# Kernel tuning notes

Hardware: AMD Instinct MI355X
Metric: run time of the kernel (lower is better)

## Reference

```python
import jax, jax.numpy as jnp
import numpy as np

N = 50000   # num_nodes
E = 800000  # num edges (COO)
T = 50      # timesteps
H = 64      # hidden_units


def setup_inputs() -> dict:
    key = jax.random.key(0)
    ks = jax.random.split(key, 16)
    s = 0.1  # weight init scale
    return {
        "features": jax.random.normal(ks[0], (1, T, N), jnp.float32),
        "index": jax.random.randint(ks[1], (E, 2), 0, N, jnp.int32),
        "value": jax.random.uniform(ks[2], (E,), jnp.float32),
        "W1_g": jax.random.normal(ks[3], (1 + H, 2 * H), jnp.float32) * s,
        "b1_g": jnp.ones((2 * H,), jnp.float32),
        "W1_c": jax.random.normal(ks[4], (1 + H, H), jnp.float32) * s,
        "b1_c": jnp.zeros((H,), jnp.float32),
        "W2b_g": jax.random.normal(ks[5], (H + 1, 2), jnp.float32) * s,
        "b2b_g": jnp.ones((2,), jnp.float32),
        "W2b_c": jax.random.normal(ks[6], (H + 1, 1), jnp.float32) * s,
        "b2b_c": jnp.zeros((1,), jnp.float32),
        "W2u_g": jax.random.normal(ks[7], (H + 1, 2), jnp.float32) * s,
        "b2u_g": jnp.ones((2,), jnp.float32),
        "W2u_c": jax.random.normal(ks[8], (H + 1, 1), jnp.float32) * s,
        "b2u_c": jnp.zeros((1,), jnp.float32),
    }


def _spmm(rows, cols, vals, X):
    # sparse COO adjacency (rows, cols, vals) @ dense X [N, d]
    return jax.ops.segment_sum(vals[:, None] * X[cols], rows, num_segments=N)


def _gru_layer(xs, rows, cols, vals, Wg, bg, Wc, bc, units):
    # xs: [T, N, d_in]; GCN-GRU cell scanned over time, batch=1
    h0 = jnp.zeros((N, units), xs.dtype)

    def step(h, x):
        def gconv(st, W, b):
            xc = jnp.concatenate([x, st], axis=-1)     # [N, d_in+units]
            return _spmm(rows, cols, vals, xc) @ W + b  # [N, out]

        ru = jax.nn.sigmoid(gconv(h, Wg, bg))
        r, u = jnp.split(ru, 2, axis=-1)
        c = jnp.tanh(gconv(r * h, Wc, bc))
        hn = u * h + (1.0 - u) * c
        return hn, hn

    _, hs = jax.lax.scan(step, h0, xs)
    return hs  # [T, N, units]


def reference(features, index, value, W1_g, b1_g, W1_c, b1_c,
              W2b_g, b2b_g, W2b_c, b2b_c, W2u_g, b2u_g, W2u_c, b2u_c):
    rows, cols = index[:, 0], index[:, 1]
    xs = features[0][..., None]  # [T, N, 1]
    # shared first layer (cell_1 is used by both multi-cell stacks)
    h1 = _gru_layer(xs, rows, cols, value, W1_g, b1_g, W1_c, b1_c, H)  # [T,N,H]
    out_b = _gru_layer(h1, rows, cols, value, W2b_g, b2b_g, W2b_c, b2b_c, 1)
    out_u = _gru_layer(h1, rows, cols, value, W2u_g, b2u_g, W2u_c, b2u_c, 1)
    # dynamic_rnn outputs: [batch=1, T, N]
    return out_b[..., 0][None], out_u[..., 0][None]
```

## Files before the change

kernel.cpp:

```cpp
#include <hip/hip_runtime.h>
#include <math.h>

#define NN 50000
#define EE 800000
#define TT 50
#define EVCAP 1150016
#define SB 196

__device__ __forceinline__ float sigm(float x)   { return 1.f / (1.f + __expf(-x)); }
__device__ __forceinline__ float tanh_f(float x) { float e = __expf(2.f * x); return 1.f - 2.f / (e + 1.f); }


__global__ __launch_bounds__(256) void hist_kernel(const int* __restrict__ idx, int* __restrict__ cnt) {
    int e = blockIdx.x * blockDim.x + threadIdx.x;
    if (e < EE) atomicAdd(&cnt[idx[2 * e]], 1);
}

__global__ __launch_bounds__(256) void scan1(const int* __restrict__ cnt, int* __restrict__ rp,
                                             int* __restrict__ bsum) {
    __shared__ int s[256];
    int t = threadIdx.x;
    int g = blockIdx.x * 256 + t;
    int v = (g < NN) ? ((cnt[g] + 7) & ~7) : 0;
    s[t] = v;
    __syncthreads();
    for (int off = 1; off < 256; off <<= 1) {
        int add = (t >= off) ? s[t - off] : 0;
        __syncthreads();
        v += add;
        s[t] = v;
        __syncthreads();
    }
    if (g < NN) rp[g + 1] = v;
    if (t == 255) bsum[blockIdx.x] = v;
}

__global__ __launch_bounds__(256) void scan2(int* __restrict__ bsum) {
    __shared__ int s[256];
    int t = threadIdx.x;
    int v = (t < SB) ? bsum[t] : 0;
    s[t] = v;
    __syncthreads();
    for (int off = 1; off < 256; off <<= 1) {
        int add = (t >= off) ? s[t - off] : 0;
        __syncthreads();
        v += add;
        s[t] = v;
        __syncthreads();
    }
    if (t < SB) bsum[t] = v;
}

__global__ __launch_bounds__(256) void scan3(int* __restrict__ rp, const int* __restrict__ bsum) {
    int g = blockIdx.x * 256 + threadIdx.x;
    int off = (blockIdx.x > 0) ? bsum[blockIdx.x - 1] : 0;
    if (g < NN) rp[g + 1] += off;
    if (g == 0) rp[0] = 0;
}

__global__ __launch_bounds__(256) void scatter_kernel(const int* __restrict__ idx, const float* __restrict__ val,
                                                      const int* __restrict__ rp, int* __restrict__ cnt,
                                                      int2* __restrict__ ev) {
    int e = blockIdx.x * blockDim.x + threadIdx.x;
    if (e >= EE) return;
    int r = idx[2 * e];
    int p = rp[r] + atomicAdd(&cnt[r], 1);
    ev[p] = make_int2(idx[2 * e + 1], __float_as_int(val[e]));
}


__global__ __launch_bounds__(256) void transpose_x(const float* __restrict__ F, float* __restrict__ xT) {
    __shared__ float tile[64][51];
    int n0 = blockIdx.x * 64;
    for (int i = threadIdx.x; i < TT * 64; i += 256) {
        int t = i >> 6, n = i & 63;
        if (n0 + n < NN) tile[n][t] = F[(size_t)t * NN + n0 + n];
    }
    __syncthreads();
    for (int i = threadIdx.x; i < 64 * 64; i += 256) {
        int n = i >> 6, t = i & 63;
        if (n0 + n < NN) xT[(size_t)(n0 + n) * 64 + t] = (t < TT) ? tile[n][t] : 0.f;
    }
}

__global__ __launch_bounds__(256) void spmm_sx(const int* __restrict__ rp, const int2* __restrict__ ev,
                                               const float* __restrict__ xT, float* __restrict__ SxAll) {
    int w = __builtin_amdgcn_readfirstlane((blockIdx.x * blockDim.x + threadIdx.x) >> 6);
    int lane = threadIdx.x & 63;
    if (w >= NN) return;
    int e  = __builtin_amdgcn_readfirstlane(rp[w]);
    int e1 = __builtin_amdgcn_readfirstlane(rp[w + 1]);
    const float* xl = xT + lane;
    float a0 = 0.f, a1 = 0.f, a2 = 0.f, a3 = 0.f, a4 = 0.f, a5 = 0.f, a6 = 0.f, a7 = 0.f;
    for (; e < e1; e += 8) {
        int2 q0 = ev[e + 0], q1 = ev[e + 1], q2 = ev[e + 2], q3 = ev[e + 3];
        int2 q4 = ev[e + 4], q5 = ev[e + 5], q6 = ev[e + 6], q7 = ev[e + 7];
        a0 = fmaf(__int_as_float(q0.y), xl[(size_t)q0.x * 64], a0);
        a1 = fmaf(__int_as_float(q1.y), xl[(size_t)q1.x * 64], a1);
        a2 = fmaf(__int_as_float(q2.y), xl[(size_t)q2.x * 64], a2);
        a3 = fmaf(__int_as_float(q3.y), xl[(size_t)q3.x * 64], a3);
        a4 = fmaf(__int_as_float(q4.y), xl[(size_t)q4.x * 64], a4);
        a5 = fmaf(__int_as_float(q5.y), xl[(size_t)q5.x * 64], a5);
        a6 = fmaf(__int_as_float(q6.y), xl[(size_t)q6.x * 64], a6);
        a7 = fmaf(__int_as_float(q7.y), xl[(size_t)q7.x * 64], a7);
    }
    float s = ((a0 + a1) + (a2 + a3)) + ((a4 + a5) + (a6 + a7));
    if (lane < TT) SxAll[(size_t)lane * NN + w] = s;
}


__global__ __launch_bounds__(256) void spmm_cand(const int* __restrict__ rp, const int2* __restrict__ ev,
        const float* __restrict__ rh, const float* __restrict__ Sx,
        const float* __restrict__ Wc, const float* __restrict__ bc,
        const float* __restrict__ u1, float* __restrict__ h1,
        const float* __restrict__ Wbg, const float* __restrict__ Wbc,
        const float* __restrict__ Wug, const float* __restrict__ Wuc,
        float* __restrict__ z8) {
    __shared__ float ldsW[65 * 64];
    __shared__ float ldsS[4][64];
    int t = threadIdx.x;
    for (int i = t; i < 65 * 16; i += 256)
        ((float4*)ldsW)[i] = ((const float4*)Wc)[i];
    __syncthreads();
    int lane = t & 63;
    int wv = t >> 6;
    int j = lane;
    float bj = bc[j];
    float wz0 = Wbg[j * 2], wz1 = Wbg[j * 2 + 1], wz2 = Wbc[j];
    float wz3 = Wug[j * 2], wz4 = Wug[j * 2 + 1], wz5 = Wuc[j];
    int wstride = gridDim.x * 4;
    for (int wi = blockIdx.x * 4 + wv; wi < NN; wi += wstride) {
        int w = __builtin_amdgcn_readfirstlane(wi);
        int e  = __builtin_amdgcn_readfirstlane(rp[w]);
        int e1 = __builtin_amdgcn_readfirstlane(rp[w + 1]);
        const float* xl = rh + lane;
        float a0 = 0.f, a1 = 0.f, a2 = 0.f, a3 = 0.f, a4 = 0.f, a5 = 0.f, a6 = 0.f, a7 = 0.f;
        for (; e < e1; e += 8) {
            int2 q0 = ev[e + 0], q1 = ev[e + 1], q2 = ev[e + 2], q3 = ev[e + 3];
            int2 q4 = ev[e + 4], q5 = ev[e + 5], q6 = ev[e + 6], q7 = ev[e + 7];
            a0 = fmaf(__int_as_float(q0.y), xl[(size_t)q0.x * 64], a0);
            a1 = fmaf(__int_as_float(q1.y), xl[(size_t)q1.x * 64], a1);
            a2 = fmaf(__int_as_float(q2.y), xl[(size_t)q2.x * 64], a2);
            a3 = fmaf(__int_as_float(q3.y), xl[(size_t)q3.x * 64], a3);
            a4 = fmaf(__int_as_float(q4.y), xl[(size_t)q4.x * 64], a4);
            a5 = fmaf(__int_as_float(q5.y), xl[(size_t)q5.x * 64], a5);
            a6 = fmaf(__int_as_float(q6.y), xl[(size_t)q6.x * 64], a6);
            a7 = fmaf(__int_as_float(q7.y), xl[(size_t)q7.x * 64], a7);
        }
        float s2 = ((a0 + a1) + (a2 + a3)) + ((a4 + a5) + (a6 + a7));
        ldsS[wv][lane] = s2;
        float acc = fmaf(Sx[w], ldsW[j], bj);
#pragma unroll 8
        for (int k = 0; k < 64; ++k)
            acc = fmaf(ldsS[wv][k], ldsW[(k + 1) * 64 + j], acc);
        float c = tanh_f(acc);
        float u  = u1[(size_t)w * 64 + j];
        float ho = h1[(size_t)w * 64 + j];
        float hn = fmaf(u, ho - c, c);
        h1[(size_t)w * 64 + j] = hn;
        float p0 = hn * wz0, p1 = hn * wz1, p2 = hn * wz2;
        float p3 = hn * wz3, p4 = hn * wz4, p5 = hn * wz5;
#pragma unroll
        for (int off = 1; off < 64; off <<= 1) {
            p0 += __shfl_xor(p0, off);
            p1 += __shfl_xor(p1, off);
            p2 += __shfl_xor(p2, off);
            p3 += __shfl_xor(p3, off);
            p4 += __shfl_xor(p4, off);
            p5 += __shfl_xor(p5, off);
        }
        if (j == 0) {
            z8[(size_t)w * 8 + 0] = p0; z8[(size_t)w * 8 + 1] = p1; z8[(size_t)w * 8 + 2] = p2;
            z8[(size_t)w * 8 + 3] = p3; z8[(size_t)w * 8 + 4] = p4; z8[(size_t)w * 8 + 5] = p5;
        }
    }
}


__global__ __launch_bounds__(256) void merged1(int GA,
        const int* __restrict__ rp, const int2* __restrict__ ev,
        const float* __restrict__ h1, float* __restrict__ Sh,
        const float* __restrict__ z8,
        const float* __restrict__ hb, const float* __restrict__ hu,
        const float* __restrict__ Wbg, const float* __restrict__ bbg,
        const float* __restrict__ Wug, const float* __restrict__ bug,
        float* __restrict__ z2, float* __restrict__ g2, float* __restrict__ S3c) {
    if ((int)blockIdx.x < GA) {
        int w = __builtin_amdgcn_readfirstlane(((int)blockIdx.x * 256 + (int)threadIdx.x) >> 6);
        int lane = threadIdx.x & 63;
        if (w >= NN) return;
        int e  = __builtin_amdgcn_readfirstlane(rp[w]);
        int e1 = __builtin_amdgcn_readfirstlane(rp[w + 1]);
        const float* xl = h1 + lane;
        float a0 = 0.f, a1 = 0.f, a2 = 0.f, a3 = 0.f, a4 = 0.f, a5 = 0.f, a6 = 0.f, a7 = 0.f;
        for (; e < e1; e += 8) {
            int2 q0 = ev[e + 0], q1 = ev[e + 1], q2 = ev[e + 2], q3 = ev[e + 3];
            int2 q4 = ev[e + 4], q5 = ev[e + 5], q6 = ev[e + 6], q7 = ev[e + 7];
            a0 = fmaf(__int_as_float(q0.y), xl[(size_t)q0.x * 64], a0);
            a1 = fmaf(__int_as_float(q1.y), xl[(size_t)q1.x * 64], a1);
            a2 = fmaf(__int_as_float(q2.y), xl[(size_t)q2.x * 64], a2);
            a3 = fmaf(__int_as_float(q3.y), xl[(size_t)q3.x * 64], a3);
            a4 = fmaf(__int_as_float(q4.y), xl[(size_t)q4.x * 64], a4);
            a5 = fmaf(__int_as_float(q5.y), xl[(size_t)q5.x * 64], a5);
            a6 = fmaf(__int_as_float(q6.y), xl[(size_t)q6.x * 64], a6);
            a7 = fmaf(__int_as_float(q7.y), xl[(size_t)q7.x * 64], a7);
        }
        Sh[(size_t)w * 64 + lane] = ((a0 + a1) + (a2 + a3)) + ((a4 + a5) + (a6 + a7));
    } else {
        int gid = ((int)blockIdx.x - GA) * 256 + threadIdx.x;
        int row = gid >> 3;
        int j = gid & 7;
        if (row >= NN) return;
        int e = rp[row], e1 = rp[row + 1];
        float a0 = 0.f, a1 = 0.f, a2 = 0.f, a3 = 0.f;
        for (; e + 3 < e1; e += 4) {
            int2 p0 = ev[e], p1 = ev[e + 1], p2 = ev[e + 2], p3 = ev[e + 3];
            a0 = fmaf(__int_as_float(p0.y), z8[(size_t)p0.x * 8 + j], a0);
            a1 = fmaf(__int_as_float(p1.y), z8[(size_t)p1.x * 8 + j], a1);
            a2 = fmaf(__int_as_float(p2.y), z8[(size_t)p2.x * 8 + j], a2);
            a3 = fmaf(__int_as_float(p3.y), z8[(size_t)p3.x * 8 + j], a3);
        }
        for (; e < e1; ++e) {
            int2 p = ev[e];
            a0 = fmaf(__int_as_float(p.y), z8[(size_t)p.x * 8 + j], a0);
        }
        float s = (a0 + a1) + (a2 + a3);
        if (j == 2) S3c[row * 2 + 0] = s;
        if (j == 5) S3c[row * 2 + 1] = s;
        int lane = threadIdx.x & 63;
        int base = lane & ~7;
        float s0 = __shfl(s, base + 0);
        float s1 = __shfl(s, base + 1);
        float s3 = __shfl(s, base + 3);
        float s4 = __shfl(s, base + 4);
        float s6 = __shfl(s, base + 6);
        float s7 = __shfl(s, base + 7);
        if (j == 0) {
            float rb = sigm(fmaf(s6, Wbg[128], s0) + bbg[0]);
            float ub = sigm(fmaf(s6, Wbg[129], s1) + bbg[1]);
            float ru = sigm(fmaf(s7, Wug[128], s3) + bug[0]);
            float uu = sigm(fmaf(s7, Wug[129], s4) + bug[1]);
            z2[row * 2 + 0] = rb * hb[row];
            z2[row * 2 + 1] = ru * hu[row];
            g2[row * 2 + 0] = ub;
            g2[row * 2 + 1] = uu;
        }
    }
}


#define G1_CHUNK 32
__global__ __launch_bounds__(128) void merged2(int GA,
        const float* __restrict__ Sh, const float* __restrict__ Sx,
        const float* __restrict__ Wg, const float* __restrict__ bg,
        const float* __restrict__ h1, float* __restrict__ rh, float* __restrict__ u1,
        const int* __restrict__ rp, const int2* __restrict__ ev,
        const float* __restrict__ z2, const float* __restrict__ S3c, const float* __restrict__ g2,
        const float* __restrict__ Wbc, const float* __restrict__ bbc,
        const float* __restrict__ Wuc, const float* __restrict__ buc,
        float* __restrict__ hb, float* __restrict__ hu,
        float* __restrict__ z8, float* __restrict__ out, int tPrev) {
    __shared__ float4 s4[G1_CHUNK][16];
    __shared__ float sxl[G1_CHUNK];
    if ((int)blockIdx.x < GA) {
        int j = threadIdx.x;
        float w0 = Wg[j];
        float wk[64];
#pragma unroll
        for (int k = 0; k < 64; ++k) wk[k] = Wg[(1 + k) * 128 + j];
        float bj = bg[j];
        int n0 = (int)blockIdx.x * G1_CHUNK;
        int nmax = min(G1_CHUNK, NN - n0);
        for (int idx = j; idx < G1_CHUNK * 16; idx += 128) {
            int n = idx >> 4, q = idx & 15;
            if (n < nmax) s4[n][q] = *(const float4*)(Sh + (size_t)(n0 + n) * 64 + q * 4);
        }
        if (j < G1_CHUNK && j < nmax) sxl[j] = Sx[n0 + j];
        __syncthreads();
        for (int n = 0; n < nmax; ++n) {
            float acc = fmaf(sxl[n], w0, bj);
#pragma unroll
            for (int q = 0; q < 16; ++q) {
                float4 sv = s4[n][q];
                acc = fmaf(sv.x, wk[4 * q + 0], acc);
                acc = fmaf(sv.y, wk[4 * q + 1], acc);
                acc = fmaf(sv.z, wk[4 * q + 2], acc);
                acc = fmaf(sv.w, wk[4 * q + 3], acc);
            }
            float g = sigm(acc);
            int node = n0 + n;
            if (j < 64) rh[(size_t)node * 64 + j] = g * h1[(size_t)node * 64 + j];
            else        u1[(size_t)node * 64 + (j - 64)] = g;
        }
    } else {
        int gid = ((int)blockIdx.x - GA) * 128 + threadIdx.x;
        int row = gid >> 1;
        int j = gid & 1;
        if (row >= NN) return;
        int e = rp[row], e1 = rp[row + 1];
        float a0 = 0.f, a1 = 0.f, a2 = 0.f, a3 = 0.f;
        for (; e + 3 < e1; e += 4) {
            int2 p0 = ev[e], p1 = ev[e + 1], p2 = ev[e + 2], p3 = ev[e + 3];
            a0 = fmaf(__int_as_float(p0.y), z2[(size_t)p0.x * 2 + j], a0);
            a1 = fmaf(__int_as_float(p1.y), z2[(size_t)p1.x * 2 + j], a1);
            a2 = fmaf(__int_as_float(p2.y), z2[(size_t)p2.x * 2 + j], a2);
            a3 = fmaf(__int_as_float(p3.y), z2[(size_t)p3.x * 2 + j], a3);
        }
        for (; e < e1; ++e) {
            int2 p = ev[e];
            a0 = fmaf(__int_as_float(p.y), z2[(size_t)p.x * 2 + j], a0);
        }
        float s = (a0 + a1) + (a2 + a3);
        int lane = threadIdx.x & 63;
        int base = lane & ~1;
        float sA = __shfl(s, base + 0);
        float sB = __shfl(s, base + 1);
        if (j == 0) {
            float cb = tanh_f(fmaf(sA, Wbc[64], S3c[row * 2 + 0]) + bbc[0]);
            float cu = tanh_f(fmaf(sB, Wuc[64], S3c[row * 2 + 1]) + buc[0]);
            float ub = g2[row * 2 + 0], uu = g2[row * 2 + 1];
            float hbn = fmaf(ub, hb[row] - cb, cb);
            float hun = fmaf(uu, hu[row] - cu, cu);
            hb[row] = hbn; hu[row] = hun;
            z8[(size_t)row * 8 + 6] = hbn;
            z8[(size_t)row * 8 + 7] = hun;
            out[(size_t)tPrev * NN + row] = hbn;
            out[(size_t)(TT + tPrev) * NN + row] = hun;
        }
    }
}


extern "C" void kernel_launch(void* const* d_in, const int* in_sizes, int n_in,
                              void* d_out, int out_size, void* d_ws, size_t ws_size,
                              hipStream_t stream) {
    const float* features = (const float*)d_in[0];
    const int*   index    = (const int*)d_in[1];
    const float* value    = (const float*)d_in[2];
    const float* W1g  = (const float*)d_in[3];
    const float* b1g  = (const float*)d_in[4];
    const float* W1c  = (const float*)d_in[5];
    const float* b1c  = (const float*)d_in[6];
    const float* W2bg = (const float*)d_in[7];
    const float* b2bg = (const float*)d_in[8];
    const float* W2bc = (const float*)d_in[9];
    const float* b2bc = (const float*)d_in[10];
    const float* W2ug = (const float*)d_in[11];
    const float* b2ug = (const float*)d_in[12];
    const float* W2uc = (const float*)d_in[13];
    const float* b2uc = (const float*)d_in[14];
    float* out = (float*)d_out;

    char* ws = (char*)d_ws;
    size_t o = 0;
    auto alloc = [&](size_t bytes) { size_t cur = o; o += (bytes + 255) & ~(size_t)255; return cur; };
    size_t o_h1  = alloc((size_t)NN * 64 * 4);
    size_t o_hb  = alloc((size_t)NN * 4);
    size_t o_hu  = alloc((size_t)NN * 4);
    size_t o_z8  = alloc((size_t)NN * 8 * 4);
    size_t zeroEnd = o;
    size_t o_rp  = alloc((size_t)(NN + 1) * 4);
    size_t o_cnt = alloc((size_t)NN * 4);
    size_t o_bs  = alloc((size_t)256 * 4);
    size_t o_ev  = alloc((size_t)EVCAP * 8);
    size_t o_Sh  = alloc((size_t)NN * 64 * 4);
    size_t o_SxA = alloc((size_t)TT * NN * 4);
    size_t o_rh  = alloc((size_t)NN * 64 * 4);
    size_t o_u1  = alloc((size_t)NN * 64 * 4);
    size_t o_S3c = alloc((size_t)NN * 2 * 4);
    size_t o_z2  = alloc((size_t)NN * 2 * 4);
    size_t o_g2  = alloc((size_t)NN * 2 * 4);
    (void)ws_size; (void)in_sizes; (void)n_in; (void)out_size;

    float* h1  = (float*)(ws + o_h1);
    float* hb  = (float*)(ws + o_hb);
    float* hu  = (float*)(ws + o_hu);
    float* z8  = (float*)(ws + o_z8);
    int*   rp  = (int*)(ws + o_rp);
    int*   cnt = (int*)(ws + o_cnt);
    int*   bsum = (int*)(ws + o_bs);
    int2*  ev  = (int2*)(ws + o_ev);
    float* Sh  = (float*)(ws + o_Sh);
    float* SxA = (float*)(ws + o_SxA);
    float* rh  = (float*)(ws + o_rh);
    float* u1  = (float*)(ws + o_u1);
    float* S3c = (float*)(ws + o_S3c);
    float* z2  = (float*)(ws + o_z2);
    float* g2  = (float*)(ws + o_g2);
    float* xT  = rh;

    (void)hipMemsetAsync(ws + o_cnt, 0, (size_t)NN * 4, stream);
    hist_kernel<<<(EE + 255) / 256, 256, 0, stream>>>(index, cnt);
    scan1<<<SB, 256, 0, stream>>>(cnt, rp, bsum);
    scan2<<<1, 256, 0, stream>>>(bsum);
    scan3<<<SB, 256, 0, stream>>>(rp, bsum);
    (void)hipMemsetAsync(ws + o_cnt, 0, (size_t)NN * 4, stream);
    (void)hipMemsetAsync(ws + o_ev, 0, (size_t)EVCAP * 8, stream);
    scatter_kernel<<<(EE + 255) / 256, 256, 0, stream>>>(index, value, rp, cnt, ev);

    (void)hipMemsetAsync(ws + o_h1, 0, zeroEnd - o_h1, stream);
    (void)hipMemsetAsync(ws + o_Sh, 0, (size_t)NN * 64 * 4, stream);

    transpose_x<<<(NN + 63) / 64, 256, 0, stream>>>(features, xT);
    spmm_sx<<<(NN + 3) / 4, 256, 0, stream>>>(rp, ev, xT, SxA);

    const int GA1 = (NN + 3) / 4;
    const int GB1 = (NN * 8 + 255) / 256;
    const int GA2 = (NN + G1_CHUNK - 1) / G1_CHUNK;
    const int GB2 = (NN * 2 + 127) / 128;

    for (int t = 0; t < TT; ++t) {
        const float* Sxt = SxA + (size_t)t * NN;
        int g2grid = (t > 0) ? (GA2 + GB2) : GA2;
        merged2<<<g2grid, 128, 0, stream>>>(GA2, Sh, Sxt, W1g, b1g, h1, rh, u1,
                                            rp, ev, z2, S3c, g2, W2bc, b2bc, W2uc, b2uc,
                                            hb, hu, z8, out, t - 1);
        spmm_cand<<<2048, 256, 0, stream>>>(rp, ev, rh, Sxt, W1c, b1c, u1, h1,
                                            W2bg, W2bc, W2ug, W2uc, z8);
        int gA = (t < TT - 1) ? GA1 : 0;
        merged1<<<gA + GB1, 256, 0, stream>>>(gA, rp, ev, h1, Sh,
                                              z8, hb, hu, W2bg, b2bg, W2ug, b2ug, z2, g2, S3c);
    }
    merged2<<<GB2, 128, 0, stream>>>(0, Sh, SxA, W1g, b1g, h1, rh, u1,
                                     rp, ev, z2, S3c, g2, W2bc, b2bc, W2uc, b2uc,
                                     hb, hu, z8, out, TT - 1);
}
```

Before: 6.255 ms.

## Unroll gathers to 16 edges and restructure gate GEMV to persistent 256-thread blocks

```diff
diff --git a/kernel.cpp b/kernel.cpp
--- a/kernel.cpp
+++ b/kernel.cpp
@@ -83,6 +83,45 @@
     }
 }
 
+#define GATH16(TBL)                                                                   \
+    float a0=0.f,a1=0.f,a2=0.f,a3=0.f,a4=0.f,a5=0.f,a6=0.f,a7=0.f;                    \
+    float b0=0.f,b1=0.f,b2=0.f,b3=0.f,b4=0.f,b5=0.f,b6=0.f,b7=0.f;                    \
+    for (; e + 16 <= e1; e += 16) {                                                   \
+        int2 q0=ev[e+0],q1=ev[e+1],q2=ev[e+2],q3=ev[e+3];                             \
+        int2 q4=ev[e+4],q5=ev[e+5],q6=ev[e+6],q7=ev[e+7];                             \
+        int2 r0=ev[e+8],r1=ev[e+9],r2=ev[e+10],r3=ev[e+11];                           \
+        int2 r4=ev[e+12],r5=ev[e+13],r6=ev[e+14],r7=ev[e+15];                         \
+        a0=fmaf(__int_as_float(q0.y),TBL[(size_t)q0.x*64],a0);                        \
+        a1=fmaf(__int_as_float(q1.y),TBL[(size_t)q1.x*64],a1);                        \
+        a2=fmaf(__int_as_float(q2.y),TBL[(size_t)q2.x*64],a2);                        \
+        a3=fmaf(__int_as_float(q3.y),TBL[(size_t)q3.x*64],a3);                        \
+        a4=fmaf(__int_as_float(q4.y),TBL[(size_t)q4.x*64],a4);                        \
+        a5=fmaf(__int_as_float(q5.y),TBL[(size_t)q5.x*64],a5);                        \
+        a6=fmaf(__int_as_float(q6.y),TBL[(size_t)q6.x*64],a6);                        \
+        a7=fmaf(__int_as_float(q7.y),TBL[(size_t)q7.x*64],a7);                        \
+        b0=fmaf(__int_as_float(r0.y),TBL[(size_t)r0.x*64],b0);                        \
+        b1=fmaf(__int_as_float(r1.y),TBL[(size_t)r1.x*64],b1);                        \
+        b2=fmaf(__int_as_float(r2.y),TBL[(size_t)r2.x*64],b2);                        \
+        b3=fmaf(__int_as_float(r3.y),TBL[(size_t)r3.x*64],b3);                        \
+        b4=fmaf(__int_as_float(r4.y),TBL[(size_t)r4.x*64],b4);                        \
+        b5=fmaf(__int_as_float(r5.y),TBL[(size_t)r5.x*64],b5);                        \
+        b6=fmaf(__int_as_float(r6.y),TBL[(size_t)r6.x*64],b6);                        \
+        b7=fmaf(__int_as_float(r7.y),TBL[(size_t)r7.x*64],b7);                        \
+    }                                                                                 \
+    if (e < e1) {                                                 \
+        int2 q0=ev[e+0],q1=ev[e+1],q2=ev[e+2],q3=ev[e+3];                             \
+        int2 q4=ev[e+4],q5=ev[e+5],q6=ev[e+6],q7=ev[e+7];                             \
+        a0=fmaf(__int_as_float(q0.y),TBL[(size_t)q0.x*64],a0);                        \
+        a1=fmaf(__int_as_float(q1.y),TBL[(size_t)q1.x*64],a1);                        \
+        a2=fmaf(__int_as_float(q2.y),TBL[(size_t)q2.x*64],a2);                        \
+        a3=fmaf(__int_as_float(q3.y),TBL[(size_t)q3.x*64],a3);                        \
+        a4=fmaf(__int_as_float(q4.y),TBL[(size_t)q4.x*64],a4);                        \
+        a5=fmaf(__int_as_float(q5.y),TBL[(size_t)q5.x*64],a5);                        \
+        a6=fmaf(__int_as_float(q6.y),TBL[(size_t)q6.x*64],a6);                        \
+        a7=fmaf(__int_as_float(q7.y),TBL[(size_t)q7.x*64],a7);                        \
+    }                                                                                 \
+    float rsum = (((a0+a1)+(a2+a3))+((a4+a5)+(a6+a7))) + (((b0+b1)+(b2+b3))+((b4+b5)+(b6+b7)));
+
 __global__ __launch_bounds__(256) void spmm_sx(const int* __restrict__ rp, const int2* __restrict__ ev,
                                                const float* __restrict__ xT, float* __restrict__ SxAll) {
     int w = __builtin_amdgcn_readfirstlane((blockIdx.x * blockDim.x + threadIdx.x) >> 6);
@@ -91,21 +130,8 @@
     int e  = __builtin_amdgcn_readfirstlane(rp[w]);
     int e1 = __builtin_amdgcn_readfirstlane(rp[w + 1]);
     const float* xl = xT + lane;
-    float a0 = 0.f, a1 = 0.f, a2 = 0.f, a3 = 0.f, a4 = 0.f, a5 = 0.f, a6 = 0.f, a7 = 0.f;
-    for (; e < e1; e += 8) {
-        int2 q0 = ev[e + 0], q1 = ev[e + 1], q2 = ev[e + 2], q3 = ev[e + 3];
-        int2 q4 = ev[e + 4], q5 = ev[e + 5], q6 = ev[e + 6], q7 = ev[e + 7];
-        a0 = fmaf(__int_as_float(q0.y), xl[(size_t)q0.x * 64], a0);
-        a1 = fmaf(__int_as_float(q1.y), xl[(size_t)q1.x * 64], a1);
-        a2 = fmaf(__int_as_float(q2.y), xl[(size_t)q2.x * 64], a2);
-        a3 = fmaf(__int_as_float(q3.y), xl[(size_t)q3.x * 64], a3);
-        a4 = fmaf(__int_as_float(q4.y), xl[(size_t)q4.x * 64], a4);
-        a5 = fmaf(__int_as_float(q5.y), xl[(size_t)q5.x * 64], a5);
-        a6 = fmaf(__int_as_float(q6.y), xl[(size_t)q6.x * 64], a6);
-        a7 = fmaf(__int_as_float(q7.y), xl[(size_t)q7.x * 64], a7);
-    }
-    float s = ((a0 + a1) + (a2 + a3)) + ((a4 + a5) + (a6 + a7));
-    if (lane < TT) SxAll[(size_t)lane * NN + w] = s;
+    GATH16(xl)
+    if (lane < TT) SxAll[(size_t)lane * NN + w] = rsum;
 }
 
 
@@ -134,21 +160,8 @@
         int e  = __builtin_amdgcn_readfirstlane(rp[w]);
         int e1 = __builtin_amdgcn_readfirstlane(rp[w + 1]);
         const float* xl = rh + lane;
-        float a0 = 0.f, a1 = 0.f, a2 = 0.f, a3 = 0.f, a4 = 0.f, a5 = 0.f, a6 = 0.f, a7 = 0.f;
-        for (; e < e1; e += 8) {
-            int2 q0 = ev[e + 0], q1 = ev[e + 1], q2 = ev[e + 2], q3 = ev[e + 3];
-            int2 q4 = ev[e + 4], q5 = ev[e + 5], q6 = ev[e + 6], q7 = ev[e + 7];
-            a0 = fmaf(__int_as_float(q0.y), xl[(size_t)q0.x * 64], a0);
-            a1 = fmaf(__int_as_float(q1.y), xl[(size_t)q1.x * 64], a1);
-            a2 = fmaf(__int_as_float(q2.y), xl[(size_t)q2.x * 64], a2);
-            a3 = fmaf(__int_as_float(q3.y), xl[(size_t)q3.x * 64], a3);
-            a4 = fmaf(__int_as_float(q4.y), xl[(size_t)q4.x * 64], a4);
-            a5 = fmaf(__int_as_float(q5.y), xl[(size_t)q5.x * 64], a5);
-            a6 = fmaf(__int_as_float(q6.y), xl[(size_t)q6.x * 64], a6);
-            a7 = fmaf(__int_as_float(q7.y), xl[(size_t)q7.x * 64], a7);
-        }
-        float s2 = ((a0 + a1) + (a2 + a3)) + ((a4 + a5) + (a6 + a7));
-        ldsS[wv][lane] = s2;
+        GATH16(xl)
+        ldsS[wv][lane] = rsum;
         float acc = fmaf(Sx[w], ldsW[j], bj);
 #pragma unroll 8
         for (int k = 0; k < 64; ++k)
@@ -192,39 +205,28 @@
         int e  = __builtin_amdgcn_readfirstlane(rp[w]);
         int e1 = __builtin_amdgcn_readfirstlane(rp[w + 1]);
         const float* xl = h1 + lane;
-        float a0 = 0.f, a1 = 0.f, a2 = 0.f, a3 = 0.f, a4 = 0.f, a5 = 0.f, a6 = 0.f, a7 = 0.f;
-        for (; e < e1; e += 8) {
-            int2 q0 = ev[e + 0], q1 = ev[e + 1], q2 = ev[e + 2], q3 = ev[e + 3];
-            int2 q4 = ev[e + 4], q5 = ev[e + 5], q6 = ev[e + 6], q7 = ev[e + 7];
-            a0 = fmaf(__int_as_float(q0.y), xl[(size_t)q0.x * 64], a0);
-            a1 = fmaf(__int_as_float(q1.y), xl[(size_t)q1.x * 64], a1);
-            a2 = fmaf(__int_as_float(q2.y), xl[(size_t)q2.x * 64], a2);
-            a3 = fmaf(__int_as_float(q3.y), xl[(size_t)q3.x * 64], a3);
-            a4 = fmaf(__int_as_float(q4.y), xl[(size_t)q4.x * 64], a4);
-            a5 = fmaf(__int_as_float(q5.y), xl[(size_t)q5.x * 64], a5);
-            a6 = fmaf(__int_as_float(q6.y), xl[(size_t)q6.x * 64], a6);
-            a7 = fmaf(__int_as_float(q7.y), xl[(size_t)q7.x * 64], a7);
-        }
-        Sh[(size_t)w * 64 + lane] = ((a0 + a1) + (a2 + a3)) + ((a4 + a5) + (a6 + a7));
+        GATH16(xl)
+        Sh[(size_t)w * 64 + lane] = rsum;
     } else {
         int gid = ((int)blockIdx.x - GA) * 256 + threadIdx.x;
         int row = gid >> 3;
         int j = gid & 7;
         if (row >= NN) return;
         int e = rp[row], e1 = rp[row + 1];
-        float a0 = 0.f, a1 = 0.f, a2 = 0.f, a3 = 0.f;
-        for (; e + 3 < e1; e += 4) {
+        float a0 = 0.f, a1 = 0.f, a2 = 0.f, a3 = 0.f, a4 = 0.f, a5 = 0.f, a6 = 0.f, a7 = 0.f;
+        for (; e + 7 < e1; e += 8) {
             int2 p0 = ev[e], p1 = ev[e + 1], p2 = ev[e + 2], p3 = ev[e + 3];
+            int2 p4 = ev[e + 4], p5 = ev[e + 5], p6 = ev[e + 6], p7 = ev[e + 7];
             a0 = fmaf(__int_as_float(p0.y), z8[(size_t)p0.x * 8 + j], a0);
             a1 = fmaf(__int_as_float(p1.y), z8[(size_t)p1.x * 8 + j], a1);
             a2 = fmaf(__int_as_float(p2.y), z8[(size_t)p2.x * 8 + j], a2);
             a3 = fmaf(__int_as_float(p3.y), z8[(size_t)p3.x * 8 + j], a3);
-        }
-        for (; e < e1; ++e) {
-            int2 p = ev[e];
-            a0 = fmaf(__int_as_float(p.y), z8[(size_t)p.x * 8 + j], a0);
-        }
-        float s = (a0 + a1) + (a2 + a3);
+            a4 = fmaf(__int_as_float(p4.y), z8[(size_t)p4.x * 8 + j], a4);
+            a5 = fmaf(__int_as_float(p5.y), z8[(size_t)p5.x * 8 + j], a5);
+            a6 = fmaf(__int_as_float(p6.y), z8[(size_t)p6.x * 8 + j], a6);
+            a7 = fmaf(__int_as_float(p7.y), z8[(size_t)p7.x * 8 + j], a7);
+        }
+        float s = ((a0 + a1) + (a2 + a3)) + ((a4 + a5) + (a6 + a7));
         if (j == 2) S3c[row * 2 + 0] = s;
         if (j == 5) S3c[row * 2 + 1] = s;
         int lane = threadIdx.x & 63;
@@ -249,8 +251,13 @@
 }
 
 
-#define G1_CHUNK 32
-__global__ __launch_bounds__(128) void merged2(int GA,
+#define WLOAD(q) float4 wv##q = make_float4(Wg[(4*q+1)*128+j], Wg[(4*q+2)*128+j], \
+                                            Wg[(4*q+3)*128+j], Wg[(4*q+4)*128+j])
+#define SFMA(q)  { float4 s_ = srow[q]; \
+                   acc = fmaf(s_.x, wv##q.x, acc); acc = fmaf(s_.y, wv##q.y, acc); \
+                   acc = fmaf(s_.z, wv##q.z, acc); acc = fmaf(s_.w, wv##q.w, acc); }
+
+__global__ __launch_bounds__(256) void merged2(int GA,
         const float* __restrict__ Sh, const float* __restrict__ Sx,
         const float* __restrict__ Wg, const float* __restrict__ bg,
         const float* __restrict__ h1, float* __restrict__ rh, float* __restrict__ u1,
@@ -260,57 +267,47 @@
         const float* __restrict__ Wuc, const float* __restrict__ buc,
         float* __restrict__ hb, float* __restrict__ hu,
         float* __restrict__ z8, float* __restrict__ out, int tPrev) {
-    __shared__ float4 s4[G1_CHUNK][16];
-    __shared__ float sxl[G1_CHUNK];
     if ((int)blockIdx.x < GA) {
-        int j = threadIdx.x;
+        int j = threadIdx.x & 127;
+        int g = threadIdx.x >> 7;
         float w0 = Wg[j];
-        float wk[64];
-#pragma unroll
-        for (int k = 0; k < 64; ++k) wk[k] = Wg[(1 + k) * 128 + j];
         float bj = bg[j];
-        int n0 = (int)blockIdx.x * G1_CHUNK;
-        int nmax = min(G1_CHUNK, NN - n0);
-        for (int idx = j; idx < G1_CHUNK * 16; idx += 128) {
-            int n = idx >> 4, q = idx & 15;
-            if (n < nmax) s4[n][q] = *(const float4*)(Sh + (size_t)(n0 + n) * 64 + q * 4);
-        }
-        if (j < G1_CHUNK && j < nmax) sxl[j] = Sx[n0 + j];
-        __syncthreads();
-        for (int n = 0; n < nmax; ++n) {
-            float acc = fmaf(sxl[n], w0, bj);
-#pragma unroll
-            for (int q = 0; q < 16; ++q) {
-                float4 sv = s4[n][q];
-                acc = fmaf(sv.x, wk[4 * q + 0], acc);
-                acc = fmaf(sv.y, wk[4 * q + 1], acc);
-                acc = fmaf(sv.z, wk[4 * q + 2], acc);
-                acc = fmaf(sv.w, wk[4 * q + 3], acc);
-            }
-            float g = sigm(acc);
-            int node = n0 + n;
-            if (j < 64) rh[(size_t)node * 64 + j] = g * h1[(size_t)node * 64 + j];
-            else        u1[(size_t)node * 64 + (j - 64)] = g;
+        WLOAD(0);  WLOAD(1);  WLOAD(2);  WLOAD(3);
+        WLOAD(4);  WLOAD(5);  WLOAD(6);  WLOAD(7);
+        WLOAD(8);  WLOAD(9);  WLOAD(10); WLOAD(11);
+        WLOAD(12); WLOAD(13); WLOAD(14); WLOAD(15);
+        for (int n = (int)blockIdx.x * 2 + g; n < NN; n += GA * 2) {
+            int nn = __builtin_amdgcn_readfirstlane(n);
+            const float4* srow = (const float4*)(Sh + (size_t)nn * 64);
+            float acc = fmaf(Sx[nn], w0, bj);
+            SFMA(0);  SFMA(1);  SFMA(2);  SFMA(3);
+            SFMA(4);  SFMA(5);  SFMA(6);  SFMA(7);
+            SFMA(8);  SFMA(9);  SFMA(10); SFMA(11);
+            SFMA(12); SFMA(13); SFMA(14); SFMA(15);
+            float gg = sigm(acc);
+            if (j < 64) rh[(size_t)nn * 64 + j] = gg * h1[(size_t)nn * 64 + j];
+            else        u1[(size_t)nn * 64 + (j - 64)] = gg;
         }
     } else {
-        int gid = ((int)blockIdx.x - GA) * 128 + threadIdx.x;
+        int gid = ((int)blockIdx.x - GA) * 256 + threadIdx.x;
         int row = gid >> 1;
         int j = gid & 1;
         if (row >= NN) return;
         int e = rp[row], e1 = rp[row + 1];
-        float a0 = 0.f, a1 = 0.f, a2 = 0.f, a3 = 0.f;
-        for (; e + 3 < e1; e += 4) {
+        float a0 = 0.f, a1 = 0.f, a2 = 0.f, a3 = 0.f, a4 = 0.f, a5 = 0.f, a6 = 0.f, a7 = 0.f;
+        for (; e + 7 < e1; e += 8) {
             int2 p0 = ev[e], p1 = ev[e + 1], p2 = ev[e + 2], p3 = ev[e + 3];
+            int2 p4 = ev[e + 4], p5 = ev[e + 5], p6 = ev[e + 6], p7 = ev[e + 7];
             a0 = fmaf(__int_as_float(p0.y), z2[(size_t)p0.x * 2 + j], a0);
             a1 = fmaf(__int_as_float(p1.y), z2[(size_t)p1.x * 2 + j], a1);
             a2 = fmaf(__int_as_float(p2.y), z2[(size_t)p2.x * 2 + j], a2);
             a3 = fmaf(__int_as_float(p3.y), z2[(size_t)p3.x * 2 + j], a3);
-        }
-        for (; e < e1; ++e) {
-            int2 p = ev[e];
-            a0 = fmaf(__int_as_float(p.y), z2[(size_t)p.x * 2 + j], a0);
-        }
-        float s = (a0 + a1) + (a2 + a3);
+            a4 = fmaf(__int_as_float(p4.y), z2[(size_t)p4.x * 2 + j], a4);
+            a5 = fmaf(__int_as_float(p5.y), z2[(size_t)p5.x * 2 + j], a5);
+            a6 = fmaf(__int_as_float(p6.y), z2[(size_t)p6.x * 2 + j], a6);
+            a7 = fmaf(__int_as_float(p7.y), z2[(size_t)p7.x * 2 + j], a7);
+        }
+        float s = ((a0 + a1) + (a2 + a3)) + ((a4 + a5) + (a6 + a7));
         int lane = threadIdx.x & 63;
         int base = lane & ~1;
         float sA = __shfl(s, base + 0);
@@ -406,13 +403,13 @@
 
     const int GA1 = (NN + 3) / 4;
     const int GB1 = (NN * 8 + 255) / 256;
-    const int GA2 = (NN + G1_CHUNK - 1) / G1_CHUNK;
-    const int GB2 = (NN * 2 + 127) / 128;
+    const int GA2 = 1024;
+    const int GB2 = (NN * 2 + 255) / 256;
 
     for (int t = 0; t < TT; ++t) {
         const float* Sxt = SxA + (size_t)t * NN;
         int g2grid = (t > 0) ? (GA2 + GB2) : GA2;
-        merged2<<<g2grid, 128, 0, stream>>>(GA2, Sh, Sxt, W1g, b1g, h1, rh, u1,
+        merged2<<<g2grid, 256, 0, stream>>>(GA2, Sh, Sxt, W1g, b1g, h1, rh, u1,
                                             rp, ev, z2, S3c, g2, W2bc, b2bc, W2uc, b2uc,
                                             hb, hu, z8, out, t - 1);
         spmm_cand<<<2048, 256, 0, stream>>>(rp, ev, rh, Sxt, W1c, b1c, u1, h1,
@@ -421,7 +418,7 @@
         merged1<<<gA + GB1, 256, 0, stream>>>(gA, rp, ev, h1, Sh,
                                               z8, hb, hu, W2bg, b2bg, W2ug, b2ug, z2, g2, S3c);
     }
-    merged2<<<GB2, 128, 0, stream>>>(0, Sh, SxA, W1g, b1g, h1, rh, u1,
+    merged2<<<GB2, 256, 0, stream>>>(0, Sh, SxA, W1g, b1g, h1, rh, u1,
                                      rp, ev, z2, S3c, g2, W2bc, b2bc, W2uc, b2uc,
                                      hb, hu, z8, out, TT - 1);
 }
```

Measured after the change: 6.275 ms. Within noise of the previous version (+0.3%).
